# Kernel optimization log

Measured on AMD Instinct MI355X. Metric: run time of the kernel, lower is better.

## Reference

```python
import jax, jax.numpy as jnp
import numpy as np

N_NODES = 100000
N_EDGES = 1600000
N_LABEL = 200000
HID = 128
OUT = 5


def setup_inputs() -> dict:
    key = jax.random.key(0)
    k1, k2, k3, k4, k5 = jax.random.split(key, 5)
    x = jax.random.normal(k1, (N_NODES, HID), dtype=jnp.float32)
    edge_index = jax.random.randint(k2, (2, N_EDGES), 0, N_NODES, dtype=jnp.int64)
    edge_label_index = jax.random.randint(k3, (2, N_LABEL), 0, N_NODES, dtype=jnp.int64)
    W_gcn = jax.random.normal(k4, (HID, HID), dtype=jnp.float32) / np.sqrt(HID)
    b_gcn = jnp.zeros((HID,), dtype=jnp.float32)
    W_lin = jax.random.normal(k5, (2 * HID, OUT), dtype=jnp.float32) / np.sqrt(2 * HID)
    b_lin = jnp.zeros((OUT,), dtype=jnp.float32)
    return {"x": x, "edge_index": edge_index, "edge_label_index": edge_label_index,
            "W_gcn": W_gcn, "b_gcn": b_gcn, "W_lin": W_lin, "b_lin": b_lin}


def _gcn_conv(x, edge_index, W, b):
    # PyG GCNConv defaults: add self-loops, symmetric normalization,
    # linear transform first, then scatter-add of norm * x[src] into dst.
    n = x.shape[0]
    loop = jnp.arange(n, dtype=edge_index.dtype)
    src = jnp.concatenate([edge_index[0], loop])  # [E+N]
    dst = jnp.concatenate([edge_index[1], loop])  # [E+N]
    xw = x @ W  # [N, H]
    ones = jnp.ones(src.shape[0], dtype=x.dtype)
    deg = jax.ops.segment_sum(ones, dst, num_segments=n)  # in-degree incl self-loop
    dinv = jnp.where(deg > 0, jax.lax.rsqrt(deg), 0.0)
    norm = dinv[src] * dinv[dst]  # [E+N]
    msgs = xw[src] * norm[:, None]  # [E+N, H] gather + scale
    out = jax.ops.segment_sum(msgs, dst, num_segments=n)  # scatter-add
    return out + b


def reference(x, edge_index, edge_label_index, W_gcn, b_gcn, W_lin, b_lin):
    h = _gcn_conv(x, edge_index, W_gcn, b_gcn)  # [N, H]
    drug_emb = h[edge_label_index[0]]  # [E_label, H]
    prot_emb = h[edge_label_index[1]]  # [E_label, H]
    edge_emb = jnp.concatenate([drug_emb, prot_emb], axis=1)  # [E_label, 2H]
    return edge_emb @ W_lin + b_lin  # [E_label, OUT]
```

## Files before the change

### kernel.cpp

```cpp
#include <hip/hip_runtime.h>

#define N_NODES 100000
#define N_EDGES 1600000
#define N_LABEL 200000
#define HID 128
#define OUT 5

#define NBUCK 391
#define EPB   2048
#define NBLK_E 782


__global__ __launch_bounds__(256) void k_precomp(const float* __restrict__ Wg,
                                                 const float* __restrict__ bg,
                                                 const float* __restrict__ Wl,
                                                 float* __restrict__ G) {
    int o = blockIdx.x * 256 + threadIdx.x;
    if (o >= 129 * 16) return;
    int r = o >> 4, jj = o & 15;
    float acc = 0.f;
    if (jj < 2 * OUT) {
        const int half = (jj >= OUT);
        const int j = half ? jj - OUT : jj;
        for (int c = 0; c < HID; ++c) {
            float w2 = Wl[(half * HID + c) * OUT + j];
            float a = (r < HID) ? Wg[r * HID + c] : bg[c];
            acc += a * w2;
        }
    }
    G[o] = acc;
}

__global__ __launch_bounds__(256) void k_hist(const int* __restrict__ ei,
                                              int* __restrict__ hist) {
    __shared__ int h[NBUCK];
    const int t = threadIdx.x, b = blockIdx.x;
    for (int i = t; i < NBUCK; i += 256) h[i] = 0;
    __syncthreads();
    const int e0 = b * EPB;
#pragma unroll
    for (int i = 0; i < 8; ++i) {
        int e = e0 + i * 256 + t;
        if (e < N_EDGES) atomicAdd(&h[ei[N_EDGES + e] >> 8], 1);
    }
    __syncthreads();
    for (int i = t; i < NBUCK; i += 256) hist[i * NBLK_E + b] = h[i];
}

__global__ __launch_bounds__(256) void k_scanb(int* __restrict__ hist,
                                               int* __restrict__ btot) {
    __shared__ int part[256];
    const int b = blockIdx.x, t = threadIdx.x;
    int* row = hist + b * NBLK_E;
    const int lo = t * 4, hi = min(lo + 4, NBLK_E);
    int v[4]; int s = 0;
    for (int i = lo; i < hi; ++i) { v[i - lo] = row[i]; s += v[i - lo]; }
    part[t] = s;
    __syncthreads();
#pragma unroll
    for (int off = 1; off < 256; off <<= 1) {
        int a = (t >= off) ? part[t - off] : 0;
        __syncthreads();
        part[t] += a;
        __syncthreads();
    }
    int run = part[t] - s;
    for (int i = lo; i < hi; ++i) { int x = v[i - lo]; row[i] = run; run += x; }
    if (t == 255) btot[b] = part[255];
}

__global__ __launch_bounds__(512) void k_base(const int* __restrict__ btot,
                                              int* __restrict__ bbase) {
    __shared__ int part[512];
    const int t = threadIdx.x;
    int v = (t < NBUCK) ? btot[t] : 0;
    part[t] = v;
    __syncthreads();
#pragma unroll
    for (int off = 1; off < 512; off <<= 1) {
        int a = (t >= off) ? part[t - off] : 0;
        __syncthreads();
        part[t] += a;
        __syncthreads();
    }
    if (t < NBUCK) bbase[t] = part[t] - v;
    if (t == 511) bbase[NBUCK] = part[511];
}

__global__ __launch_bounds__(256) void k_part(const int* __restrict__ ei,
                                              const int* __restrict__ hist,
                                              const int* __restrict__ bbase,
                                              unsigned* __restrict__ bedge) {
    __shared__ int cur[NBUCK];
    const int t = threadIdx.x, b = blockIdx.x;
    for (int i = t; i < NBUCK; i += 256) cur[i] = bbase[i] + hist[i * NBLK_E + b];
    __syncthreads();
    const int e0 = b * EPB;
#pragma unroll
    for (int i = 0; i < 8; ++i) {
        int e = e0 + i * 256 + t;
        if (e < N_EDGES) {
            int dst = ei[N_EDGES + e];
            unsigned src = (unsigned)ei[e];
            int pos = atomicAdd(&cur[dst >> 8], 1);
            bedge[pos] = src | ((unsigned)(dst & 255) << 20);
        }
    }
}

__global__ __launch_bounds__(256) void k_build(const unsigned* __restrict__ bedge,
                                               const int* __restrict__ bbase,
                                               int* __restrict__ csr,
                                               int2* __restrict__ seg,
                                               float* __restrict__ dinv) {
    __shared__ int cnt[256];
    __shared__ int nb[256];
    __shared__ int cursor[256];
    const int b = blockIdx.x, t = threadIdx.x;
    const int base = bbase[b];
    const int size = bbase[b + 1] - base;
    cnt[t] = 0;
    __syncthreads();
    for (int i = t; i < size; i += 256) atomicAdd(&cnt[bedge[base + i] >> 20], 1);
    __syncthreads();
    const int c = cnt[t];
    nb[t] = c;
    __syncthreads();
#pragma unroll
    for (int off = 1; off < 256; off <<= 1) {
        int a = (t >= off) ? nb[t - off] : 0;
        __syncthreads();
        nb[t] += a;
        __syncthreads();
    }
    const int myBase = nb[t] - c;
    cursor[t] = myBase;
    __syncthreads();
    for (int i = t; i < size; i += 256) {
        unsigned v = bedge[base + i];
        int pos = atomicAdd(&cursor[v >> 20], 1);
        csr[base + pos] = (int)(v & 0xFFFFFu);
    }
    const int n = b * 256 + t;
    if (n < N_NODES) {
        seg[n] = make_int2(base + myBase, c);
        dinv[n] = rsqrtf((float)(c + 1));
    }
}

__global__ __launch_bounds__(256) void k_t(const float* __restrict__ x,
                                           const float* __restrict__ G,
                                           const float* __restrict__ dinv,
                                           float* __restrict__ t) {
    __shared__ float Gs[HID * 11];
    const int tid = threadIdx.x;
    for (int o = tid; o < HID * 10; o += 256) {
        int k = o / 10, j = o - k * 10;
        Gs[k * 11 + j] = G[k * 16 + j];
    }
    __syncthreads();

    int gid = blockIdx.x * 256 + tid;
    int n = gid >> 4;
    int i = gid & 15;

    float xv[8];
#pragma unroll
    for (int m = 0; m < 8; ++m) xv[m] = x[(size_t)n * HID + i + 16 * m];

    float p[10];
#pragma unroll
    for (int j = 0; j < 10; ++j) p[j] = 0.f;
#pragma unroll
    for (int m = 0; m < 8; ++m) {
        const float* g = &Gs[(i + 16 * m) * 11];
#pragma unroll
        for (int j = 0; j < 10; ++j) p[j] += xv[m] * g[j];
    }
#pragma unroll
    for (int off = 1; off < 16; off <<= 1) {
#pragma unroll
        for (int j = 0; j < 10; ++j) p[j] += __shfl_xor(p[j], off);
    }
    float val = (i == 0) ? p[0] : (i == 1) ? p[1] : (i == 2) ? p[2] : (i == 3) ? p[3] :
                (i == 4) ? p[4] : (i == 5) ? p[5] : (i == 6) ? p[6] : (i == 7) ? p[7] :
                (i == 8) ? p[8] : (i == 9) ? p[9] : 0.f;
    t[(size_t)n * 16 + i] = dinv[n] * val;
}

__global__ __launch_bounds__(256) void k_pullt(const float* __restrict__ t,
                                               const int2* __restrict__ seg,
                                               const int* __restrict__ csr,
                                               const float* __restrict__ dinv,
                                               const float* __restrict__ G,
                                               float* __restrict__ proj) {
    int gid = blockIdx.x * 256 + threadIdx.x;
    int n = gid >> 4;
    int i = gid & 15;
    const int gbase = threadIdx.x & 48;

    float acc = t[(size_t)n * 16 + i];
    const int2 sg = seg[n];
    const int beg = sg.x, deg = sg.y;

    for (int base = 0; base < deg; base += 16) {
        const int cnt = min(16, deg - base);
        int idx = (i < cnt) ? csr[beg + base + i] : 0;
        int j = 0;
        for (; j + 4 <= cnt; j += 4) {
            int s0 = __shfl(idx, gbase + j);
            int s1 = __shfl(idx, gbase + j + 1);
            int s2 = __shfl(idx, gbase + j + 2);
            int s3 = __shfl(idx, gbase + j + 3);
            float v0 = t[(size_t)s0 * 16 + i];
            float v1 = t[(size_t)s1 * 16 + i];
            float v2 = t[(size_t)s2 * 16 + i];
            float v3 = t[(size_t)s3 * 16 + i];
            acc += v0; acc += v1; acc += v2; acc += v3;
        }
        for (; j < cnt; ++j) {
            int s = __shfl(idx, gbase + j);
            acc += t[(size_t)s * 16 + i];
        }
    }
    proj[(size_t)n * 16 + i] = dinv[n] * acc + G[HID * 16 + i];
}

__global__ __launch_bounds__(256) void k_link2(const int* __restrict__ eli,
                                               const float* __restrict__ proj,
                                               const float* __restrict__ bl,
                                               float* __restrict__ out) {
    int t = blockIdx.x * 256 + threadIdx.x;
    int l = t >> 3, o = t & 7;
    if (l >= N_LABEL || o >= OUT) return;
    int d = eli[l];
    int p = eli[N_LABEL + l];
    out[l * OUT + o] = proj[d * 16 + o] + proj[p * 16 + OUT + o] + bl[o];
}

extern "C" void kernel_launch(void* const* d_in, const int* in_sizes, int n_in,
                              void* d_out, int out_size, void* d_ws, size_t ws_size,
                              hipStream_t stream) {
    const float* x     = (const float*)d_in[0];
    const int*   ei    = (const int*)d_in[1];
    const int*   eli   = (const int*)d_in[2];
    const float* W_gcn = (const float*)d_in[3];
    const float* b_gcn = (const float*)d_in[4];
    const float* W_lin = (const float*)d_in[5];
    const float* b_lin = (const float*)d_in[6];
    float* out = (float*)d_out;

    float* t         = (float*)d_ws;
    float* proj      = t + (size_t)N_NODES * 16;
    float* G         = proj + (size_t)N_NODES * 16;
    float* dinv      = G + 129 * 16;
    unsigned* bedge  = (unsigned*)(dinv + N_NODES);
    int*   csr       = (int*)(bedge + N_EDGES);
    int2*  seg       = (int2*)(csr + N_EDGES);
    int*   hist      = (int*)(seg + N_NODES);
    int*   btot      = hist + NBUCK * NBLK_E;
    int*   bbase     = btot + NBUCK;

    k_precomp<<<(129 * 16 + 255) / 256, 256, 0, stream>>>(W_gcn, b_gcn, W_lin, G);
    k_hist<<<NBLK_E, 256, 0, stream>>>(ei, hist);
    k_scanb<<<NBUCK, 256, 0, stream>>>(hist, btot);
    k_base<<<1, 512, 0, stream>>>(btot, bbase);
    k_part<<<NBLK_E, 256, 0, stream>>>(ei, hist, bbase, bedge);
    k_build<<<NBUCK, 256, 0, stream>>>(bedge, bbase, csr, seg, dinv);
    k_t<<<N_NODES * 16 / 256, 256, 0, stream>>>(x, G, dinv, t);
    k_pullt<<<N_NODES * 16 / 256, 256, 0, stream>>>(t, seg, csr, dinv, G, proj);
    k_link2<<<(N_LABEL * 8 + 255) / 256, 256, 0, stream>>>(eli, proj, b_lin, out);
}
```

Measured before the change: 115.6 us.

## Store projected features as bf16, widen pull to a wavefront per node, merge launches

Packs the per-node 10-wide projected features into bf16 pairs, halving the bytes each gathered neighbor row costs. The pull kernel now gives each node a full 64-lane wavefront that processes 8 edges in parallel, followed by a shuffle reduction. The weight precompute is folded into extra blocks of the histogram kernel. The separate bucket-base scan is replaced by an atomic counter, so bucket order becomes nondeterministic but stays contiguous. Bf16 rounding adds precision loss to the aggregation, and the memset adds one launch.

```diff
diff --git a/kernel.cpp b/kernel.cpp
--- a/kernel.cpp
+++ b/kernel.cpp
@@ -9,32 +9,46 @@
 #define NBUCK 391
 #define EPB   2048
 #define NBLK_E 782
-
-
-__global__ __launch_bounds__(256) void k_precomp(const float* __restrict__ Wg,
-                                                 const float* __restrict__ bg,
-                                                 const float* __restrict__ Wl,
-                                                 float* __restrict__ G) {
-    int o = blockIdx.x * 256 + threadIdx.x;
-    if (o >= 129 * 16) return;
-    int r = o >> 4, jj = o & 15;
-    float acc = 0.f;
-    if (jj < 2 * OUT) {
-        const int half = (jj >= OUT);
-        const int j = half ? jj - OUT : jj;
-        for (int c = 0; c < HID; ++c) {
-            float w2 = Wl[(half * HID + c) * OUT + j];
-            float a = (r < HID) ? Wg[r * HID + c] : bg[c];
-            acc += a * w2;
+#define PREC_BLKS 9
+
+
+__device__ inline void bf2x(unsigned u, float& lo, float& hi) {
+    lo = __uint_as_float(u << 16);
+    hi = __uint_as_float(u & 0xffff0000u);
+}
+__device__ inline unsigned pack2(float a, float b) {
+    unsigned ua = __float_as_uint(a), ub = __float_as_uint(b);
+    ua = (ua + 0x7fffu + ((ua >> 16) & 1u)) >> 16;
+    ub = (ub + 0x7fffu + ((ub >> 16) & 1u)) & 0xffff0000u;
+    return ua | ub;
+}
+
+__global__ __launch_bounds__(256) void k_hist(const int* __restrict__ ei,
+                                              int* __restrict__ hist,
+                                              const float* __restrict__ Wg,
+                                              const float* __restrict__ bg,
+                                              const float* __restrict__ Wl,
+                                              float* __restrict__ G) {
+    const int t = threadIdx.x, b = blockIdx.x;
+    if (b >= NBLK_E) {
+        int o = (b - NBLK_E) * 256 + t;
+        if (o < 129 * 16) {
+            int r = o >> 4, jj = o & 15;
+            float acc = 0.f;
+            if (jj < 2 * OUT) {
+                const int half = (jj >= OUT);
+                const int j = half ? jj - OUT : jj;
+                for (int c = 0; c < HID; ++c) {
+                    float w2 = Wl[(half * HID + c) * OUT + j];
+                    float a = (r < HID) ? Wg[r * HID + c] : bg[c];
+                    acc += a * w2;
+                }
+            }
+            G[o] = acc;
         }
-    }
-    G[o] = acc;
-}
-
-__global__ __launch_bounds__(256) void k_hist(const int* __restrict__ ei,
-                                              int* __restrict__ hist) {
+        return;
+    }
     __shared__ int h[NBUCK];
-    const int t = threadIdx.x, b = blockIdx.x;
     for (int i = t; i < NBUCK; i += 256) h[i] = 0;
     __syncthreads();
     const int e0 = b * EPB;
@@ -48,7 +62,9 @@
 }
 
 __global__ __launch_bounds__(256) void k_scanb(int* __restrict__ hist,
-                                               int* __restrict__ btot) {
+                                               int* __restrict__ btot,
+                                               int* __restrict__ bbase,
+                                               int* __restrict__ total) {
     __shared__ int part[256];
     const int b = blockIdx.x, t = threadIdx.x;
     int* row = hist + b * NBLK_E;
@@ -66,25 +82,11 @@
     }
     int run = part[t] - s;
     for (int i = lo; i < hi; ++i) { int x = v[i - lo]; row[i] = run; run += x; }
-    if (t == 255) btot[b] = part[255];
-}
-
-__global__ __launch_bounds__(512) void k_base(const int* __restrict__ btot,
-                                              int* __restrict__ bbase) {
-    __shared__ int part[512];
-    const int t = threadIdx.x;
-    int v = (t < NBUCK) ? btot[t] : 0;
-    part[t] = v;
-    __syncthreads();
-#pragma unroll
-    for (int off = 1; off < 512; off <<= 1) {
-        int a = (t >= off) ? part[t - off] : 0;
-        __syncthreads();
-        part[t] += a;
-        __syncthreads();
-    }
-    if (t < NBUCK) bbase[t] = part[t] - v;
-    if (t == 511) bbase[NBUCK] = part[511];
+    if (t == 255) {
+        int tot = part[255];
+        btot[b] = tot;
+        bbase[b] = atomicAdd(total, tot);
+    }
 }
 
 __global__ __launch_bounds__(256) void k_part(const int* __restrict__ ei,
@@ -110,6 +112,7 @@
 
 __global__ __launch_bounds__(256) void k_build(const unsigned* __restrict__ bedge,
                                                const int* __restrict__ bbase,
+                                               const int* __restrict__ btot,
                                                int* __restrict__ csr,
                                                int2* __restrict__ seg,
                                                float* __restrict__ dinv) {
@@ -118,7 +121,7 @@
     __shared__ int cursor[256];
     const int b = blockIdx.x, t = threadIdx.x;
     const int base = bbase[b];
-    const int size = bbase[b + 1] - base;
+    const int size = btot[b];
     cnt[t] = 0;
     __syncthreads();
     for (int i = t; i < size; i += 256) atomicAdd(&cnt[bedge[base + i] >> 20], 1);
@@ -151,7 +154,7 @@
 __global__ __launch_bounds__(256) void k_t(const float* __restrict__ x,
                                            const float* __restrict__ G,
                                            const float* __restrict__ dinv,
-                                           float* __restrict__ t) {
+                                           unsigned* __restrict__ t16) {
     __shared__ float Gs[HID * 11];
     const int tid = threadIdx.x;
     for (int o = tid; o < HID * 10; o += 256) {
@@ -182,48 +185,60 @@
 #pragma unroll
         for (int j = 0; j < 10; ++j) p[j] += __shfl_xor(p[j], off);
     }
-    float val = (i == 0) ? p[0] : (i == 1) ? p[1] : (i == 2) ? p[2] : (i == 3) ? p[3] :
-                (i == 4) ? p[4] : (i == 5) ? p[5] : (i == 6) ? p[6] : (i == 7) ? p[7] :
-                (i == 8) ? p[8] : (i == 9) ? p[9] : 0.f;
-    t[(size_t)n * 16 + i] = dinv[n] * val;
-}
-
-__global__ __launch_bounds__(256) void k_pullt(const float* __restrict__ t,
+    float va = (i == 0) ? p[0] : (i == 1) ? p[2] : (i == 2) ? p[4] : (i == 3) ? p[6] : p[8];
+    float vb = (i == 0) ? p[1] : (i == 1) ? p[3] : (i == 2) ? p[5] : (i == 3) ? p[7] : p[9];
+    float di = dinv[n];
+    if (i < 5)      t16[(size_t)n * 8 + i] = pack2(di * va, di * vb);
+    else if (i < 8) t16[(size_t)n * 8 + i] = 0u;
+}
+
+__global__ __launch_bounds__(256) void k_pullt(const unsigned* __restrict__ t16,
                                                const int2* __restrict__ seg,
                                                const int* __restrict__ csr,
                                                const float* __restrict__ dinv,
                                                const float* __restrict__ G,
                                                float* __restrict__ proj) {
-    int gid = blockIdx.x * 256 + threadIdx.x;
-    int n = gid >> 4;
-    int i = gid & 15;
-    const int gbase = threadIdx.x & 48;
-
-    float acc = t[(size_t)n * 16 + i];
+    const int gid = blockIdx.x * 256 + threadIdx.x;
+    const int n = gid >> 6;
+    const int lane = gid & 63;
+    const int e2 = lane >> 3;
+    const int i = lane & 7;
+
+    float aLo = 0.f, aHi = 0.f;
+    if (e2 == 0) {
+        bf2x(t16[(size_t)n * 8 + i], aLo, aHi);
+    }
+
     const int2 sg = seg[n];
     const int beg = sg.x, deg = sg.y;
 
-    for (int base = 0; base < deg; base += 16) {
-        const int cnt = min(16, deg - base);
-        int idx = (i < cnt) ? csr[beg + base + i] : 0;
-        int j = 0;
-        for (; j + 4 <= cnt; j += 4) {
-            int s0 = __shfl(idx, gbase + j);
-            int s1 = __shfl(idx, gbase + j + 1);
-            int s2 = __shfl(idx, gbase + j + 2);
-            int s3 = __shfl(idx, gbase + j + 3);
-            float v0 = t[(size_t)s0 * 16 + i];
-            float v1 = t[(size_t)s1 * 16 + i];
-            float v2 = t[(size_t)s2 * 16 + i];
-            float v3 = t[(size_t)s3 * 16 + i];
-            acc += v0; acc += v1; acc += v2; acc += v3;
+    for (int base = 0; base < deg; base += 64) {
+        const int cnt = min(64, deg - base);
+        int myIdx = (lane < cnt) ? csr[beg + base + lane] : 0;
+#pragma unroll
+        for (int j = 0; j < 8; ++j) {
+            int e = j * 8 + e2;
+            int s = __shfl(myIdx, e);
+            unsigned u = 0u;
+            if (e < cnt) u = t16[(size_t)s * 8 + i];
+            float lo, hi;
+            bf2x(u, lo, hi);
+            aLo += lo; aHi += hi;
         }
-        for (; j < cnt; ++j) {
-            int s = __shfl(idx, gbase + j);
-            acc += t[(size_t)s * 16 + i];
-        }
-    }
-    proj[(size_t)n * 16 + i] = dinv[n] * acc + G[HID * 16 + i];
+    }
+
+    aLo += __shfl_xor(aLo, 8);  aHi += __shfl_xor(aHi, 8);
+    aLo += __shfl_xor(aLo, 16); aHi += __shfl_xor(aHi, 16);
+    aLo += __shfl_xor(aLo, 32); aHi += __shfl_xor(aHi, 32);
+
+    if (lane < 5) {
+        float di = dinv[n];
+        float2 c0 = ((const float2*)(G + HID * 16))[lane];
+        float2 r;
+        r.x = di * aLo + c0.x;
+        r.y = di * aHi + c0.y;
+        *(float2*)&proj[(size_t)n * 16 + 2 * lane] = r;
+    }
 }
 
 __global__ __launch_bounds__(256) void k_link2(const int* __restrict__ eli,
@@ -250,8 +265,8 @@
     const float* b_lin = (const float*)d_in[6];
     float* out = (float*)d_out;
 
-    float* t         = (float*)d_ws;
-    float* proj      = t + (size_t)N_NODES * 16;
+    unsigned* t16    = (unsigned*)d_ws;
+    float* proj      = (float*)(t16 + (size_t)N_NODES * 8);
     float* G         = proj + (size_t)N_NODES * 16;
     float* dinv      = G + 129 * 16;
     unsigned* bedge  = (unsigned*)(dinv + N_NODES);
@@ -260,14 +275,15 @@
     int*   hist      = (int*)(seg + N_NODES);
     int*   btot      = hist + NBUCK * NBLK_E;
     int*   bbase     = btot + NBUCK;
-
-    k_precomp<<<(129 * 16 + 255) / 256, 256, 0, stream>>>(W_gcn, b_gcn, W_lin, G);
-    k_hist<<<NBLK_E, 256, 0, stream>>>(ei, hist);
-    k_scanb<<<NBUCK, 256, 0, stream>>>(hist, btot);
-    k_base<<<1, 512, 0, stream>>>(btot, bbase);
+    int*   total     = bbase + NBUCK;
+
+    hipMemsetAsync(total, 0, sizeof(int), stream);
+
+    k_hist<<<NBLK_E + PREC_BLKS, 256, 0, stream>>>(ei, hist, W_gcn, b_gcn, W_lin, G);
+    k_scanb<<<NBUCK, 256, 0, stream>>>(hist, btot, bbase, total);
     k_part<<<NBLK_E, 256, 0, stream>>>(ei, hist, bbase, bedge);
-    k_build<<<NBUCK, 256, 0, stream>>>(bedge, bbase, csr, seg, dinv);
-    k_t<<<N_NODES * 16 / 256, 256, 0, stream>>>(x, G, dinv, t);
-    k_pullt<<<N_NODES * 16 / 256, 256, 0, stream>>>(t, seg, csr, dinv, G, proj);
+    k_build<<<NBUCK, 256, 0, stream>>>(bedge, bbase, btot, csr, seg, dinv);
+    k_t<<<N_NODES * 16 / 256, 256, 0, stream>>>(x, G, dinv, t16);
+    k_pullt<<<N_NODES * 64 / 256, 256, 0, stream>>>(t16, seg, csr, dinv, G, proj);
     k_link2<<<(N_LABEL * 8 + 255) / 256, 256, 0, stream>>>(eli, proj, b_lin, out);
 }
```

Measured after the change: 126.0 us. +9.0%, slower.
